# Kernel tuning notes

Measured on AMD Instinct MI355X. Metric: run time of the kernel, lower is better.

The kernel has to match this reference:

```python
import jax, jax.numpy as jnp
import numpy as np

DIM, NH, NKV, HD = 4096, 32, 8, 128
B, KV_LEN, WINDOW = 32, 4096, 4096
G = NH // NKV  # q heads per kv head (GQA group)


def setup_inputs() -> dict:
    key = jax.random.key(0)
    ks = jax.random.split(key, 7)
    s = 1.0 / np.sqrt(DIM)
    return {
        "x": jax.random.normal(ks[0], (1, 1, B, DIM), jnp.float32),
        "wqkv": jax.random.normal(ks[1], (DIM, DIM + 2 * NKV * HD), jnp.float32) * s,
        "wo": jax.random.normal(ks[2], (DIM, DIM), jnp.float32) * s,
        "rot_mat": jax.random.normal(ks[3], (HD, HD), jnp.float32) * (1.0 / np.sqrt(HD)),
        "cache_k": jax.random.normal(ks[4], (B, NKV, KV_LEN, HD), jnp.float32),
        "cache_v": jax.random.normal(ks[5], (B, NKV, KV_LEN, HD), jnp.float32),
        "attn_mask": jnp.zeros((1, NH, B, WINDOW), jnp.float32),
        "current_pos": 4095,
    }


def reference(x, wqkv, wo, rot_mat, cache_k, cache_v, attn_mask, current_pos):
    # fused QKV projection: (1,1,B,DIM) @ (DIM,6144) -> (1,1,B,6144)
    xqkv = x @ wqkv
    q = xqkv[..., : NH * HD].reshape(1, 1, B, NH, HD)
    k = xqkv[..., NH * HD : (NH + NKV) * HD].reshape(1, 1, B, NKV, HD)
    v = xqkv[..., (NH + NKV) * HD :].reshape(1, 1, B, NKV, HD)
    # nlp_create_qkv_heads layout: (seq, n_heads, batch, head_dim)
    q = jnp.transpose(q[:, 0], (0, 2, 1, 3))  # (1, NH, B, HD)
    k = jnp.transpose(k[:, 0], (0, 2, 1, 3))  # (1, NKV, B, HD)
    v = jnp.transpose(v[:, 0], (0, 2, 1, 3))  # (1, NKV, B, HD)
    # RoPE as matmul on last dim
    q = q @ rot_mat
    k = k @ rot_mat
    # KV-cache update at current_pos: cache is (B, NKV, KV_LEN, HD)
    cache_k = cache_k.at[:, :, current_pos, :].set(jnp.transpose(k[0], (1, 0, 2)))
    cache_v = cache_v.at[:, :, current_pos, :].set(jnp.transpose(v[0], (1, 0, 2)))
    # unpad valid region (padded to nearest 32, capped by sliding window)
    L = min(((current_pos + 1 + 31) // 32) * 32, WINDOW)
    keys = cache_k[:, :, :L]    # (B, NKV, L, HD)
    values = cache_v[:, :, :L]  # (B, NKV, L, HD)
    # grouped attention: q (1, NKV, G, B, HD) vs keys (B, NKV, L, HD)
    qg = q.reshape(1, NKV, G, B, HD)
    scores = jnp.einsum("qkgbd,bkld->qkgbl", qg, keys)  # (1,NKV,G,B,L)
    scores = scores.reshape(1, NH, B, L) / jnp.sqrt(jnp.float32(HD))
    scores = scores + attn_mask[..., :L]
    probs = jax.nn.softmax(scores, axis=-1)
    out = jnp.einsum("qkgbl,bkld->qkgbd", probs.reshape(1, NKV, G, B, L), values)
    out = out.reshape(1, NH, B, HD)
    # concatenate heads -> (1,1,B,DIM)
    out = jnp.transpose(out, (0, 2, 1, 3)).reshape(1, 1, B, NH * HD)
    return out @ wo
```

## Files before the change

kernel.cpp:

```cpp
#include <hip/hip_runtime.h>

#define BB 32
#define DIM 4096
#define NH 32
#define NKV 8
#define HD 128
#define KVLEN 4096
#define QKVC 6144
#define GQ 4
#define QKV_SPLITS 32
#define WO_SPLITS 32

__global__ __launch_bounds__(256, 4) void k_qkv(const float* __restrict__ x,
                                                const float* __restrict__ w,
                                                float* __restrict__ part) {
    int j  = blockIdx.x * 256 + threadIdx.x;
    int d0 = blockIdx.y * (DIM / QKV_SPLITS);
    float acc[BB];
#pragma unroll
    for (int b = 0; b < BB; ++b) acc[b] = 0.f;
    for (int dd = d0; dd < d0 + DIM / QKV_SPLITS; dd += 8) {
        float wr[8];
#pragma unroll
        for (int k = 0; k < 8; ++k) wr[k] = w[(size_t)(dd + k) * QKVC + j];
#pragma unroll
        for (int b = 0; b < BB; ++b) {
            float4 xa = *(const float4*)&x[b * DIM + dd];
            float4 xb = *(const float4*)&x[b * DIM + dd + 4];
            float t = acc[b];
            t = fmaf(xa.x, wr[0], t); t = fmaf(xa.y, wr[1], t);
            t = fmaf(xa.z, wr[2], t); t = fmaf(xa.w, wr[3], t);
            t = fmaf(xb.x, wr[4], t); t = fmaf(xb.y, wr[5], t);
            t = fmaf(xb.z, wr[6], t); t = fmaf(xb.w, wr[7], t);
            acc[b] = t;
        }
    }
#pragma unroll
    for (int b = 0; b < BB; ++b)
        part[(size_t)blockIdx.y * (BB * QKVC) + (size_t)b * QKVC + j] = acc[b];
}

__global__ __launch_bounds__(256) void k_red(const float* __restrict__ src,
                                             float* __restrict__ dst,
                                             int parts, int n4) {
    int i = blockIdx.x * 256 + threadIdx.x;
    if (i >= n4) return;
    const float4* s4 = (const float4*)src;
    float4 a = s4[i];
    for (int p = 1; p < parts; ++p) {
        float4 b = s4[(size_t)p * n4 + i];
        a.x += b.x; a.y += b.y; a.z += b.z; a.w += b.w;
    }
    ((float4*)dst)[i] = a;
}

__global__ __launch_bounds__(128) void k_rot(const float* __restrict__ xqkv,
                                             const float* __restrict__ rot,
                                             const int* __restrict__ curpos,
                                             float* __restrict__ qws,
                                             float* __restrict__ ck,
                                             float* __restrict__ cv) {
    int c  = blockIdx.x;
    int b  = blockIdx.y;
    int dp = threadIdx.x;
    int pos = *curpos;
    const float* row = &xqkv[(size_t)b * QKVC + c * HD];
    if (c < 40) {
        float acc = 0.f;
#pragma unroll 4
        for (int d = 0; d < HD; ++d) acc = fmaf(row[d], rot[d * HD + dp], acc);
        if (c < 32) {
            qws[((size_t)b * NH + c) * HD + dp] = acc;
        } else {
            int kvh = c - 32;
            ck[(((size_t)b * NKV + kvh) * KVLEN + pos) * HD + dp] = acc;
        }
    } else {
        int kvh = c - 40;
        cv[(((size_t)b * NKV + kvh) * KVLEN + pos) * HD + dp] = row[dp];
    }
}

__global__ __launch_bounds__(256, 4) void k_qk(const float* __restrict__ ck,
                                               const float* __restrict__ qws,
                                               const float* __restrict__ mask,
                                               const int* __restrict__ curpos,
                                               float* __restrict__ scores,
                                               float2* __restrict__ stats) {
    __shared__ float Kl[64 * 132];
    __shared__ float ql[4 * 128];
    int bkv = blockIdx.x;
    int split = blockIdx.y;
    int b = bkv >> 3, kv = bkv & 7;
    int tid = threadIdx.x;
    int g = tid >> 6, lane = tid & 63;
    int pos = *curpos;
    int L = min((((pos + 1) + 31) >> 5) << 5, KVLEN);

    for (int i = tid; i < GQ * HD; i += 256)
        ql[i] = qws[((size_t)b * NH + kv * GQ) * HD + i];

    const float scale = 0.08838834764831845f;
    float m = -3.0e38f, lsum = 0.f;
    int l0 = split * 1024;
    int h = kv * GQ + g;

    const float4* Kbase = (const float4*)&ck[((size_t)bkv * KVLEN + l0) * HD];
    float4 kreg[8];
#pragma unroll
    for (int i = 0; i < 8; ++i) kreg[i] = Kbase[i * 256 + tid];

    for (int t = 0; t < 16; ++t) {
#pragma unroll
        for (int i = 0; i < 8; ++i) {
            int c4i = i * 256 + tid;
            int row = c4i >> 5, c4 = c4i & 31;
            *(float4*)&Kl[row * 132 + c4 * 4] = kreg[i];
        }
        __syncthreads();
        if (t < 15) {
            const float4* Kn = Kbase + (size_t)(t + 1) * 2048;
#pragma unroll
            for (int i = 0; i < 8; ++i) kreg[i] = Kn[i * 256 + tid];
        }
        float s = 0.f;
#pragma unroll
        for (int d4 = 0; d4 < 32; ++d4) {
            float4 kk = *(const float4*)&Kl[lane * 132 + d4 * 4];
            float4 qq = *(const float4*)&ql[g * HD + d4 * 4];
            s += kk.x * qq.x + kk.y * qq.y + kk.z * qq.z + kk.w * qq.w;
        }
        int l = l0 + t * 64 + lane;
        s = s * scale + mask[((size_t)h * BB + b) * KVLEN + l];
        if (l >= L) {
            s = -3.0e38f;
        } else {
            if (s > m) { lsum = lsum * __expf(m - s) + 1.f; m = s; }
            else       { lsum += __expf(s - m); }
        }
        scores[((size_t)(bkv * GQ + g)) * KVLEN + l] = s;
        __syncthreads();
    }
#pragma unroll
    for (int off = 32; off > 0; off >>= 1) {
        float mo = __shfl_xor(m, off);
        float lo = __shfl_xor(lsum, off);
        float M2 = fmaxf(m, mo);
        lsum = lsum * __expf(m - M2) + lo * __expf(mo - M2);
        m = M2;
    }
    if (lane == 0) stats[(bkv * GQ + g) * 4 + split] = make_float2(m, lsum);
}

__global__ void k_stats(const float2* __restrict__ stats, float2* __restrict__ mfin) {
    int i = blockIdx.x * 256 + threadIdx.x;
    if (i >= BB * NKV * GQ) return;
    float m = -3.0e38f, l = 0.f;
#pragma unroll
    for (int s = 0; s < 4; ++s) {
        float2 p = stats[i * 4 + s];
        float M2 = fmaxf(m, p.x);
        l = l * __expf(m - M2) + p.y * __expf(p.x - M2);
        m = M2;
    }
    mfin[i] = make_float2(m, l > 0.f ? 1.f / l : 0.f);
}

__global__ __launch_bounds__(512, 6) void k_pv(const float* __restrict__ cv,
                                               const float* __restrict__ scores,
                                               const float2* __restrict__ mfin,
                                               float* __restrict__ attn_part) {
    int bkv = blockIdx.x;
    int split = blockIdx.y;
    int tid = threadIdx.x;
    int d4 = tid & 31;
    int lg = tid >> 5;
    int l0 = split * 1024 + lg * 64;

    float2 ML[GQ];
#pragma unroll
    for (int g = 0; g < GQ; ++g) ML[g] = mfin[bkv * GQ + g];

    float4 acc[GQ];
#pragma unroll
    for (int g = 0; g < GQ; ++g) acc[g] = make_float4(0.f, 0.f, 0.f, 0.f);

    const float* Vg = &cv[((size_t)bkv * KVLEN + l0) * HD + d4 * 4];
    const float* Sg = &scores[(size_t)bkv * GQ * KVLEN + l0];

#pragma unroll 4
    for (int i = 0; i < 64; ++i) {
        float4 v = *(const float4*)&Vg[(size_t)i * HD];
#pragma unroll
        for (int g = 0; g < GQ; ++g) {
            float s = Sg[(size_t)g * KVLEN + i];
            float p = __expf(s - ML[g].x) * ML[g].y;
            acc[g].x = fmaf(p, v.x, acc[g].x);
            acc[g].y = fmaf(p, v.y, acc[g].y);
            acc[g].z = fmaf(p, v.z, acc[g].z);
            acc[g].w = fmaf(p, v.w, acc[g].w);
        }
    }

    __shared__ float red[16][GQ][HD];
#pragma unroll
    for (int g = 0; g < GQ; ++g) *(float4*)&red[lg][g][d4 * 4] = acc[g];
    __syncthreads();
    {
        int g2 = tid >> 7, d = tid & 127;
        float o = 0.f;
#pragma unroll
        for (int k = 0; k < 16; ++k) o += red[k][g2][d];
        int b = bkv >> 3, kv = bkv & 7;
        attn_part[(size_t)split * (BB * DIM) + (size_t)b * DIM + (kv * GQ + g2) * HD + d] = o;
    }
}

__global__ __launch_bounds__(256, 4) void k_wo(const float* __restrict__ attn,
                                               const float* __restrict__ wo,
                                               float* __restrict__ part) {
    int j  = blockIdx.x * 256 + threadIdx.x;
    int d0 = blockIdx.y * (DIM / WO_SPLITS);
    float acc[BB];
#pragma unroll
    for (int b = 0; b < BB; ++b) acc[b] = 0.f;
    for (int dd = d0; dd < d0 + DIM / WO_SPLITS; dd += 8) {
        float wr[8];
#pragma unroll
        for (int k = 0; k < 8; ++k) wr[k] = wo[(size_t)(dd + k) * DIM + j];
#pragma unroll
        for (int b = 0; b < BB; ++b) {
            float4 xa = *(const float4*)&attn[b * DIM + dd];
            float4 xb = *(const float4*)&attn[b * DIM + dd + 4];
            float t = acc[b];
            t = fmaf(xa.x, wr[0], t); t = fmaf(xa.y, wr[1], t);
            t = fmaf(xa.z, wr[2], t); t = fmaf(xa.w, wr[3], t);
            t = fmaf(xb.x, wr[4], t); t = fmaf(xb.y, wr[5], t);
            t = fmaf(xb.z, wr[6], t); t = fmaf(xb.w, wr[7], t);
            acc[b] = t;
        }
    }
#pragma unroll
    for (int b = 0; b < BB; ++b)
        part[(size_t)blockIdx.y * (BB * DIM) + (size_t)b * DIM + j] = acc[b];
}

extern "C" void kernel_launch(void* const* d_in, const int* in_sizes, int n_in,
                              void* d_out, int out_size, void* d_ws, size_t ws_size,
                              hipStream_t stream) {
    const float* x    = (const float*)d_in[0];
    const float* wqkv = (const float*)d_in[1];
    const float* wo   = (const float*)d_in[2];
    const float* rot  = (const float*)d_in[3];
    float* ck         = (float*)d_in[4];
    float* cv         = (float*)d_in[5];
    const float* mask = (const float*)d_in[6];
    const int* curpos = (const int*)d_in[7];
    float* out        = (float*)d_out;

    char* ws = (char*)d_ws;
    float*  xqkv_part = (float*)(ws);
    float*  xqkv      = (float*)(ws + 25165824);
    float*  qws       = (float*)(ws + 25952256);
    float*  scores    = (float*)(ws + 26476544);
    float2* stats     = (float2*)(ws + 43253760);
    float2* mfin      = (float2*)(ws + 43286528);
    float*  attn_part = (float*)(ws + 43294720);
    float*  attn      = (float*)(ws + 45391872);
    float*  out_part  = (float*)(ws + 45916160);

    k_qkv  <<<dim3(QKVC / 256, QKV_SPLITS), 256, 0, stream>>>(x, wqkv, xqkv_part);
    k_red  <<<dim3(192),                    256, 0, stream>>>(xqkv_part, xqkv, QKV_SPLITS, BB * QKVC / 4);
    k_rot  <<<dim3(48, BB),                 128, 0, stream>>>(xqkv, rot, curpos, qws, ck, cv);
    k_qk   <<<dim3(BB * NKV, 4),            256, 0, stream>>>(ck, qws, mask, curpos, scores, stats);
    k_stats<<<dim3(4),                      256, 0, stream>>>(stats, mfin);
    k_pv   <<<dim3(BB * NKV, 4),            512, 0, stream>>>(cv, scores, mfin, attn_part);
    k_red  <<<dim3(128),                    256, 0, stream>>>(attn_part, attn, 4, BB * DIM / 4);
    k_wo   <<<dim3(DIM / 256, WO_SPLITS),   256, 0, stream>>>(attn, wo, out_part);
    k_red  <<<dim3(128),                    256, 0, stream>>>(out_part, out, WO_SPLITS, BB * DIM / 4);
}
```

Measured before the change: 1.397 ms.

## Fuse QK and PV into flash-decoding kernel, use atomics for GEMM split-K

Merges the separate score, stats and PV kernels into one online-softmax attention kernel that keeps probabilities in shared memory, so the full score matrix is never written to and reread from global memory. A small merge kernel combines the four split partials. The projection GEMMs now reduce split-K partials with atomicAdd into zeroed outputs, which removes the separate reduction kernels and their large partial buffers. The trade-offs are atomic contention, extra memsets, and more per-tile syncs and rescaling work inside the attention loop.

```diff
diff --git a/kernel.cpp b/kernel.cpp
--- a/kernel.cpp
+++ b/kernel.cpp
@@ -8,18 +8,16 @@
 #define KVLEN 4096
 #define QKVC 6144
 #define GQ 4
-#define QKV_SPLITS 32
-#define WO_SPLITS 32
-
-__global__ __launch_bounds__(256, 4) void k_qkv(const float* __restrict__ x,
-                                                const float* __restrict__ w,
-                                                float* __restrict__ part) {
+
+__global__ __launch_bounds__(256) void k_qkv(const float* __restrict__ x,
+                                             const float* __restrict__ w,
+                                             float* __restrict__ xqkv) {
     int j  = blockIdx.x * 256 + threadIdx.x;
-    int d0 = blockIdx.y * (DIM / QKV_SPLITS);
+    int d0 = blockIdx.y * 256;
     float acc[BB];
 #pragma unroll
     for (int b = 0; b < BB; ++b) acc[b] = 0.f;
-    for (int dd = d0; dd < d0 + DIM / QKV_SPLITS; dd += 8) {
+    for (int dd = d0; dd < d0 + 256; dd += 8) {
         float wr[8];
 #pragma unroll
         for (int k = 0; k < 8; ++k) wr[k] = w[(size_t)(dd + k) * QKVC + j];
@@ -36,22 +34,7 @@
         }
     }
 #pragma unroll
-    for (int b = 0; b < BB; ++b)
-        part[(size_t)blockIdx.y * (BB * QKVC) + (size_t)b * QKVC + j] = acc[b];
-}
-
-__global__ __launch_bounds__(256) void k_red(const float* __restrict__ src,
-                                             float* __restrict__ dst,
-                                             int parts, int n4) {
-    int i = blockIdx.x * 256 + threadIdx.x;
-    if (i >= n4) return;
-    const float4* s4 = (const float4*)src;
-    float4 a = s4[i];
-    for (int p = 1; p < parts; ++p) {
-        float4 b = s4[(size_t)p * n4 + i];
-        a.x += b.x; a.y += b.y; a.z += b.z; a.w += b.w;
-    }
-    ((float4*)dst)[i] = a;
+    for (int b = 0; b < BB; ++b) atomicAdd(&xqkv[(size_t)b * QKVC + j], acc[b]);
 }
 
 __global__ __launch_bounds__(128) void k_rot(const float* __restrict__ xqkv,
@@ -81,34 +64,41 @@
     }
 }
 
-__global__ __launch_bounds__(256, 4) void k_qk(const float* __restrict__ ck,
-                                               const float* __restrict__ qws,
-                                               const float* __restrict__ mask,
-                                               const int* __restrict__ curpos,
-                                               float* __restrict__ scores,
-                                               float2* __restrict__ stats) {
+__global__ __launch_bounds__(256, 4) void k_attn(const float* __restrict__ ck,
+                                                 const float* __restrict__ cv,
+                                                 const float* __restrict__ qws,
+                                                 const float* __restrict__ mask,
+                                                 const int* __restrict__ curpos,
+                                                 float* __restrict__ opart,
+                                                 float2* __restrict__ stats) {
     __shared__ float Kl[64 * 132];
-    __shared__ float ql[4 * 128];
+    __shared__ float ql[GQ * HD];
+    __shared__ float pl[GQ * 64];
+    __shared__ float rs[GQ];
     int bkv = blockIdx.x;
     int split = blockIdx.y;
     int b = bkv >> 3, kv = bkv & 7;
     int tid = threadIdx.x;
     int g = tid >> 6, lane = tid & 63;
+    int d4 = tid & 31, sub = tid >> 5;
     int pos = *curpos;
     int L = min((((pos + 1) + 31) >> 5) << 5, KVLEN);
+    int l0 = split * 1024;
+    int h = kv * GQ + g;
+    const float scale = 0.08838834764831845f;
 
     for (int i = tid; i < GQ * HD; i += 256)
         ql[i] = qws[((size_t)b * NH + kv * GQ) * HD + i];
 
-    const float scale = 0.08838834764831845f;
-    float m = -3.0e38f, lsum = 0.f;
-    int l0 = split * 1024;
-    int h = kv * GQ + g;
-
     const float4* Kbase = (const float4*)&ck[((size_t)bkv * KVLEN + l0) * HD];
     float4 kreg[8];
 #pragma unroll
     for (int i = 0; i < 8; ++i) kreg[i] = Kbase[i * 256 + tid];
+
+    float m = -3.0e38f, lsum = 0.f;
+    float4 acc[GQ];
+#pragma unroll
+    for (int gg = 0; gg < GQ; ++gg) acc[gg] = make_float4(0.f, 0.f, 0.f, 0.f);
 
     for (int t = 0; t < 16; ++t) {
 #pragma unroll
@@ -123,108 +113,113 @@
 #pragma unroll
             for (int i = 0; i < 8; ++i) kreg[i] = Kn[i * 256 + tid];
         }
+        int l = l0 + t * 64 + lane;
+        float mk = mask[((size_t)h * BB + b) * KVLEN + l];
         float s = 0.f;
 #pragma unroll
-        for (int d4 = 0; d4 < 32; ++d4) {
-            float4 kk = *(const float4*)&Kl[lane * 132 + d4 * 4];
-            float4 qq = *(const float4*)&ql[g * HD + d4 * 4];
+        for (int dd = 0; dd < 32; ++dd) {
+            float4 kk = *(const float4*)&Kl[lane * 132 + dd * 4];
+            float4 qq = *(const float4*)&ql[g * HD + dd * 4];
             s += kk.x * qq.x + kk.y * qq.y + kk.z * qq.z + kk.w * qq.w;
         }
-        int l = l0 + t * 64 + lane;
-        s = s * scale + mask[((size_t)h * BB + b) * KVLEN + l];
-        if (l >= L) {
-            s = -3.0e38f;
-        } else {
-            if (s > m) { lsum = lsum * __expf(m - s) + 1.f; m = s; }
-            else       { lsum += __expf(s - m); }
-        }
-        scores[((size_t)(bkv * GQ + g)) * KVLEN + l] = s;
+        s = s * scale + mk;
+        if (l >= L) s = -3.0e38f;
+        float smax = s;
+#pragma unroll
+        for (int off = 32; off > 0; off >>= 1)
+            smax = fmaxf(smax, __shfl_xor(smax, off));
+        float mnew = fmaxf(m, smax);
+        float r = __expf(m - mnew);
+        float e = (l < L) ? __expf(s - mnew) : 0.f;
+        float esum = e;
+#pragma unroll
+        for (int off = 32; off > 0; off >>= 1)
+            esum += __shfl_xor(esum, off);
+        lsum = lsum * r + esum;
+        m = mnew;
+        pl[g * 64 + lane] = e;
+        if (lane == 0) rs[g] = r;
         __syncthreads();
-    }
-#pragma unroll
-    for (int off = 32; off > 0; off >>= 1) {
-        float mo = __shfl_xor(m, off);
-        float lo = __shfl_xor(lsum, off);
-        float M2 = fmaxf(m, mo);
-        lsum = lsum * __expf(m - M2) + lo * __expf(mo - M2);
-        m = M2;
+        float rg[GQ];
+#pragma unroll
+        for (int gg = 0; gg < GQ; ++gg) rg[gg] = rs[gg];
+#pragma unroll
+        for (int gg = 0; gg < GQ; ++gg) {
+            acc[gg].x *= rg[gg]; acc[gg].y *= rg[gg];
+            acc[gg].z *= rg[gg]; acc[gg].w *= rg[gg];
+        }
+        const float4* Vt = (const float4*)&cv[((size_t)bkv * KVLEN + l0 + t * 64 + sub * 8) * HD];
+#pragma unroll
+        for (int i = 0; i < 8; ++i) {
+            float4 v = Vt[i * 32 + d4];
+#pragma unroll
+            for (int gg = 0; gg < GQ; ++gg) {
+                float p = pl[gg * 64 + sub * 8 + i];
+                acc[gg].x = fmaf(p, v.x, acc[gg].x);
+                acc[gg].y = fmaf(p, v.y, acc[gg].y);
+                acc[gg].z = fmaf(p, v.z, acc[gg].z);
+                acc[gg].w = fmaf(p, v.w, acc[gg].w);
+            }
+        }
     }
     if (lane == 0) stats[(bkv * GQ + g) * 4 + split] = make_float2(m, lsum);
-}
-
-__global__ void k_stats(const float2* __restrict__ stats, float2* __restrict__ mfin) {
-    int i = blockIdx.x * 256 + threadIdx.x;
-    if (i >= BB * NKV * GQ) return;
-    float m = -3.0e38f, l = 0.f;
-#pragma unroll
-    for (int s = 0; s < 4; ++s) {
-        float2 p = stats[i * 4 + s];
-        float M2 = fmaxf(m, p.x);
-        l = l * __expf(m - M2) + p.y * __expf(p.x - M2);
-        m = M2;
-    }
-    mfin[i] = make_float2(m, l > 0.f ? 1.f / l : 0.f);
-}
-
-__global__ __launch_bounds__(512, 6) void k_pv(const float* __restrict__ cv,
-                                               const float* __restrict__ scores,
-                                               const float2* __restrict__ mfin,
-                                               float* __restrict__ attn_part) {
+
+    float* red = Kl;
+#pragma unroll
+    for (int gg = 0; gg < GQ; ++gg)
+        *(float4*)&red[(sub * GQ + gg) * HD + d4 * 4] = acc[gg];
+    __syncthreads();
+#pragma unroll
+    for (int rep = 0; rep < 2; ++rep) {
+        int idx = rep * 256 + tid;
+        int g2 = idx >> 7, d = idx & 127;
+        float o = 0.f;
+#pragma unroll
+        for (int k = 0; k < 8; ++k) o += red[(k * GQ + g2) * HD + d];
+        opart[(((size_t)split * 256 + bkv) * GQ + g2) * HD + d] = o;
+    }
+}
+
+__global__ __launch_bounds__(128) void k_merge(const float* __restrict__ opart,
+                                               const float2* __restrict__ stats,
+                                               float* __restrict__ attn) {
     int bkv = blockIdx.x;
-    int split = blockIdx.y;
-    int tid = threadIdx.x;
-    int d4 = tid & 31;
-    int lg = tid >> 5;
-    int l0 = split * 1024 + lg * 64;
-
-    float2 ML[GQ];
-#pragma unroll
-    for (int g = 0; g < GQ; ++g) ML[g] = mfin[bkv * GQ + g];
-
-    float4 acc[GQ];
-#pragma unroll
-    for (int g = 0; g < GQ; ++g) acc[g] = make_float4(0.f, 0.f, 0.f, 0.f);
-
-    const float* Vg = &cv[((size_t)bkv * KVLEN + l0) * HD + d4 * 4];
-    const float* Sg = &scores[(size_t)bkv * GQ * KVLEN + l0];
-
-#pragma unroll 4
-    for (int i = 0; i < 64; ++i) {
-        float4 v = *(const float4*)&Vg[(size_t)i * HD];
-#pragma unroll
-        for (int g = 0; g < GQ; ++g) {
-            float s = Sg[(size_t)g * KVLEN + i];
-            float p = __expf(s - ML[g].x) * ML[g].y;
-            acc[g].x = fmaf(p, v.x, acc[g].x);
-            acc[g].y = fmaf(p, v.y, acc[g].y);
-            acc[g].z = fmaf(p, v.z, acc[g].z);
-            acc[g].w = fmaf(p, v.w, acc[g].w);
-        }
-    }
-
-    __shared__ float red[16][GQ][HD];
-#pragma unroll
-    for (int g = 0; g < GQ; ++g) *(float4*)&red[lg][g][d4 * 4] = acc[g];
-    __syncthreads();
-    {
-        int g2 = tid >> 7, d = tid & 127;
+    int d = threadIdx.x;
+    int b = bkv >> 3, kv = bkv & 7;
+#pragma unroll
+    for (int g = 0; g < GQ; ++g) {
+        float2 st[4];
+        float M = -3.0e38f;
+#pragma unroll
+        for (int s = 0; s < 4; ++s) {
+            st[s] = stats[(bkv * GQ + g) * 4 + s];
+            M = fmaxf(M, st[s].x);
+        }
+        float Ltot = 0.f;
+        float w[4];
+#pragma unroll
+        for (int s = 0; s < 4; ++s) {
+            w[s] = __expf(st[s].x - M);
+            Ltot += st[s].y * w[s];
+        }
+        float inv = Ltot > 0.f ? 1.f / Ltot : 0.f;
         float o = 0.f;
 #pragma unroll
-        for (int k = 0; k < 16; ++k) o += red[k][g2][d];
-        int b = bkv >> 3, kv = bkv & 7;
-        attn_part[(size_t)split * (BB * DIM) + (size_t)b * DIM + (kv * GQ + g2) * HD + d] = o;
-    }
-}
-
-__global__ __launch_bounds__(256, 4) void k_wo(const float* __restrict__ attn,
-                                               const float* __restrict__ wo,
-                                               float* __restrict__ part) {
+        for (int s = 0; s < 4; ++s)
+            o += opart[(((size_t)s * 256 + bkv) * GQ + g) * HD + d] * (w[s] * inv);
+        attn[(size_t)b * DIM + (kv * GQ + g) * HD + d] = o;
+    }
+}
+
+__global__ __launch_bounds__(256) void k_wo(const float* __restrict__ attn,
+                                            const float* __restrict__ wo,
+                                            float* __restrict__ out) {
     int j  = blockIdx.x * 256 + threadIdx.x;
-    int d0 = blockIdx.y * (DIM / WO_SPLITS);
+    int d0 = blockIdx.y * 256;
     float acc[BB];
 #pragma unroll
     for (int b = 0; b < BB; ++b) acc[b] = 0.f;
-    for (int dd = d0; dd < d0 + DIM / WO_SPLITS; dd += 8) {
+    for (int dd = d0; dd < d0 + 256; dd += 8) {
         float wr[8];
 #pragma unroll
         for (int k = 0; k < 8; ++k) wr[k] = wo[(size_t)(dd + k) * DIM + j];
@@ -241,8 +236,7 @@
         }
     }
 #pragma unroll
-    for (int b = 0; b < BB; ++b)
-        part[(size_t)blockIdx.y * (BB * DIM) + (size_t)b * DIM + j] = acc[b];
+    for (int b = 0; b < BB; ++b) atomicAdd(&out[(size_t)b * DIM + j], acc[b]);
 }
 
 extern "C" void kernel_launch(void* const* d_in, const int* in_sizes, int n_in,
@@ -259,23 +253,18 @@
     float* out        = (float*)d_out;
 
     char* ws = (char*)d_ws;
-    float*  xqkv_part = (float*)(ws);
-    float*  xqkv      = (float*)(ws + 25165824);
-    float*  qws       = (float*)(ws + 25952256);
-    float*  scores    = (float*)(ws + 26476544);
-    float2* stats     = (float2*)(ws + 43253760);
-    float2* mfin      = (float2*)(ws + 43286528);
-    float*  attn_part = (float*)(ws + 43294720);
-    float*  attn      = (float*)(ws + 45391872);
-    float*  out_part  = (float*)(ws + 45916160);
-
-    k_qkv  <<<dim3(QKVC / 256, QKV_SPLITS), 256, 0, stream>>>(x, wqkv, xqkv_part);
-    k_red  <<<dim3(192),                    256, 0, stream>>>(xqkv_part, xqkv, QKV_SPLITS, BB * QKVC / 4);
-    k_rot  <<<dim3(48, BB),                 128, 0, stream>>>(xqkv, rot, curpos, qws, ck, cv);
-    k_qk   <<<dim3(BB * NKV, 4),            256, 0, stream>>>(ck, qws, mask, curpos, scores, stats);
-    k_stats<<<dim3(4),                      256, 0, stream>>>(stats, mfin);
-    k_pv   <<<dim3(BB * NKV, 4),            512, 0, stream>>>(cv, scores, mfin, attn_part);
-    k_red  <<<dim3(128),                    256, 0, stream>>>(attn_part, attn, 4, BB * DIM / 4);
-    k_wo   <<<dim3(DIM / 256, WO_SPLITS),   256, 0, stream>>>(attn, wo, out_part);
-    k_red  <<<dim3(128),                    256, 0, stream>>>(out_part, out, WO_SPLITS, BB * DIM / 4);
-}
+    float*  xqkv  = (float*)(ws);
+    float*  qws   = (float*)(ws + 786432);
+    float*  opart = (float*)(ws + 1310720);
+    float2* stats = (float2*)(ws + 3407872);
+    float*  attn  = (float*)(ws + 3440640);
+
+    hipMemsetAsync(xqkv, 0, 786432, stream);
+    hipMemsetAsync(out, 0, (size_t)out_size * sizeof(float), stream);
+
+    k_qkv  <<<dim3(QKVC / 256, 16), 256, 0, stream>>>(x, wqkv, xqkv);
+    k_rot  <<<dim3(48, BB),         128, 0, stream>>>(xqkv, rot, curpos, qws, ck, cv);
+    k_attn <<<dim3(BB * NKV, 4),    256, 0, stream>>>(ck, cv, qws, mask, curpos, opart, stats);
+    k_merge<<<dim3(BB * NKV),       128, 0, stream>>>(opart, stats, attn);
+    k_wo   <<<dim3(DIM / 256, 16),  256, 0, stream>>>(attn, wo, out);
+}
```

Result: slower. 1.479 ms (+5.9%).
